# Optimization experiments

Measured on AMD Instinct MI355X. Metric: run time of the kernel, lower is better.

The kernel has to match this reference:

```python
import jax, jax.numpy as jnp
import numpy as np

BN_EPS = 1e-5

def _bn(x, g, b, m, v):
    # eval-mode BatchNorm1d over channel dim of [B, C, N]
    scale = g / jnp.sqrt(v + BN_EPS)
    return (x - m[:, None]) * scale[:, None] + b[:, None]

def _conv1(W, x, b=None):
    # 1x1 Conv1d == channel matmul: W [O, C], x [B, C, N] -> [B, O, N]
    y = jnp.einsum('oc,bcn->bon', W, x)
    if b is not None:
        y = y + b[:, None]
    return y

def _sa_layer(x, wqk, wv, bv, wt, bt, g, b, m, v):
    # offset self-attention; q_conv and k_conv share weights
    xk = _conv1(wqk, x)                          # [B, D, N]
    xq = jnp.swapaxes(xk, 1, 2)                  # [B, N, D]
    xv = _conv1(wv, x, bv)                       # [B, D, N]
    energy = jnp.einsum('bnd,bdm->bnm', xq, xk)  # [B, N, N]
    attn = jax.nn.softmax(energy, axis=-1)
    attn = attn / (1e-9 + attn.sum(axis=1, keepdims=True))  # L1 renorm over dim=1
    x_r = jnp.einsum('bdn,bnm->bdm', xv, attn)   # [B, D, N]
    x_r = jax.nn.relu(_bn(_conv1(wt, x - x_r, bt), g, b, m, v))
    return x + x_r

def setup_inputs() -> dict:
    key = jax.random.key(0)
    ks = iter(jax.random.split(key, 64))
    B, Cin, N = 16, 3, 2048
    D, F, H1, OUT = 128, 1024, 512, 50
    def rn(shape, s=0.05):
        return jax.random.normal(next(ks), shape, dtype=jnp.float32) * s
    def var(shape):
        return jax.random.uniform(next(ks), shape, dtype=jnp.float32) * 0.5 + 0.5
    inp = {
        'x': jax.random.normal(next(ks), (B, Cin, N), dtype=jnp.float32),
        'w1': rn((D, Cin)), 'w2': rn((D, D)),
        'bn1_g': jnp.ones((D,)), 'bn1_b': jnp.zeros((D,)), 'bn1_m': rn((D,)), 'bn1_v': var((D,)),
        'bn2_g': jnp.ones((D,)), 'bn2_b': jnp.zeros((D,)), 'bn2_m': rn((D,)), 'bn2_v': var((D,)),
        'sa_wqk': rn((4, D, D)), 'sa_wv': rn((4, D, D)), 'sa_bv': rn((4, D)),
        'sa_wt': rn((4, D, D)), 'sa_bt': rn((4, D)),
        'sa_g': jnp.ones((4, D)), 'sa_b': jnp.zeros((4, D)), 'sa_m': rn((4, D)), 'sa_v': var((4, D)),
        'wf': rn((F, 4 * D)),
        'bnf_g': jnp.ones((F,)), 'bnf_b': jnp.zeros((F,)), 'bnf_m': rn((F,)), 'bnf_v': var((F,)),
        'ws1': rn((H1, 3 * F)), 'bs1': rn((H1,)),
        'bns1_g': jnp.ones((H1,)), 'bns1_b': jnp.zeros((H1,)), 'bns1_m': rn((H1,)), 'bns1_v': var((H1,)),
        'ws2': rn((OUT, H1)), 'bs2': rn((OUT,)),
        'bns2_g': jnp.ones((OUT,)), 'bns2_b': jnp.zeros((OUT,)), 'bns2_m': rn((OUT,)), 'bns2_v': var((OUT,)),
    }
    return inp

def reference(x, w1, w2, bn1_g, bn1_b, bn1_m, bn1_v, bn2_g, bn2_b, bn2_m, bn2_v,
              sa_wqk, sa_wv, sa_bv, sa_wt, sa_bt, sa_g, sa_b, sa_m, sa_v,
              wf, bnf_g, bnf_b, bnf_m, bnf_v,
              ws1, bs1, bns1_g, bns1_b, bns1_m, bns1_v,
              ws2, bs2, bns2_g, bns2_b, bns2_m, bns2_v):
    B, _, N = x.shape
    h = jax.nn.relu(_bn(_conv1(w1, x), bn1_g, bn1_b, bn1_m, bn1_v))
    h = jax.nn.relu(_bn(_conv1(w2, h), bn2_g, bn2_b, bn2_m, bn2_v))
    feats = []
    for i in range(4):
        h = _sa_layer(h, sa_wqk[i], sa_wv[i], sa_bv[i], sa_wt[i], sa_bt[i],
                      sa_g[i], sa_b[i], sa_m[i], sa_v[i])
        feats.append(h)
    cat = jnp.concatenate(feats, axis=1)                 # [B, 512, N]
    fused = _bn(_conv1(wf, cat), bnf_g, bnf_b, bnf_m, bnf_v)
    fused = jnp.where(fused >= 0, fused, 0.2 * fused)    # LeakyReLU(0.2)
    x_max = fused.max(axis=2)                            # [B, 1024]
    x_avg = fused.mean(axis=2)                           # [B, 1024]
    gmax = jnp.broadcast_to(x_max[:, :, None], (B, x_max.shape[1], N))
    gavg = jnp.broadcast_to(x_avg[:, :, None], (B, x_avg.shape[1], N))
    h = jnp.concatenate([fused, gmax, gavg], axis=1)     # [B, 3072, N]
    h = jax.nn.relu(_bn(_conv1(ws1, h, bs1), bns1_g, bns1_b, bns1_m, bns1_v))
    # dropout is identity in eval mode
    h = jax.nn.relu(_bn(_conv1(ws2, h, bs2), bns2_g, bns2_b, bns2_m, bns2_v))
    return h  # [B, out_channel, N]
```

## Files before the change

### kernel.cpp

```cpp
#include <hip/hip_runtime.h>
#include <cstdint>
#include <cstddef>

#define B_   16
#define N_   2048
#define D_   128
#define F_   1024
#define H1_  512
#define OUT_ 50

static constexpr float BN_EPS = 1e-5f;

typedef __attribute__((ext_vector_type(8))) short short8;
typedef __attribute__((ext_vector_type(4))) float f32x4;

__device__ inline unsigned short f2bf(float f) {
  union { float f; unsigned u; } v; v.f = f;
  unsigned r = v.u + 0x7fff + ((v.u >> 16) & 1);
  return (unsigned short)(r >> 16);
}

__device__ inline void dma16(const unsigned short* g, unsigned short* l) {
  __builtin_amdgcn_global_load_lds(
      (const __attribute__((address_space(1))) unsigned int*)g,
      (__attribute__((address_space(3))) unsigned int*)l, 16, 0, 0);
}

__global__ void foldw_k(const float* __restrict__ W, int ldW,
                        const float* __restrict__ bias,
                        const float* __restrict__ g, const float* __restrict__ bb,
                        const float* __restrict__ m, const float* __restrict__ v,
                        unsigned short* __restrict__ Wb, float* __restrict__ biasF,
                        int O, int Opad, int K) {
  long i = (long)blockIdx.x * 256 + threadIdx.x;
  if (i >= (long)Opad * K) return;
  int o = (int)(i / K), k = (int)(i % K);
  float sc = 1.f, sh = 0.f;
  if (o < O && g) { sc = g[o] * rsqrtf(v[o] + BN_EPS); sh = bb[o] - m[o] * sc; }
  float w = (o < O) ? W[(long)o * ldW + k] * sc : 0.f;
  Wb[i] = f2bf(w);
  if (k == 0 && biasF) {
    float bf = 0.f;
    if (o < O) bf = (bias ? bias[o] : 0.f) * sc + sh;
    biasF[o] = bf;
  }
}

__global__ void conv1_k(const float* __restrict__ x, const float* __restrict__ w1,
                        const float* __restrict__ g, const float* __restrict__ bb,
                        const float* __restrict__ m, const float* __restrict__ v,
                        unsigned short* __restrict__ h0b) {
  int o = threadIdx.x, n = blockIdx.x, b = blockIdx.y;
  const float* xb = x + (long)b * 3 * N_;
  float val = w1[o * 3 + 0] * xb[n] + w1[o * 3 + 1] * xb[N_ + n] + w1[o * 3 + 2] * xb[2 * N_ + n];
  float sc = g[o] * rsqrtf(v[o] + BN_EPS);
  val = val * sc + (bb[o] - m[o] * sc);
  h0b[((long)b * N_ + n) * D_ + o] = f2bf(fmaxf(val, 0.f));
}

template <int TM>
__global__ __launch_bounds__(256, 4)
void gemm_tok(const unsigned short* __restrict__ Wb, int ldW,
              const unsigned short* __restrict__ A, long sA, int ldA,
              const float* __restrict__ biasF,
              const float* __restrict__ perBO, int ldPBO,
              const float* __restrict__ res, long sRes, int ldRes,
              float* __restrict__ outF, long sOutF, int ldOutF,
              unsigned short* __restrict__ outH, long sOutH, int ldOutH,
              float* __restrict__ pmax, float* __restrict__ psum,
              int K, int act, int flags) {
  constexpr int MT = TM / 32;
  __shared__ unsigned short lAB[TM * 64 + 128 * 64];
  __shared__ float lpm[4][64], lps[4][64];
  unsigned short* lA = lAB;
  unsigned short* lB = lAB + TM * 64;
  unsigned short* lS = lAB;
  int tid = threadIdx.x;
  int n0 = blockIdx.x * TM, o0 = blockIdx.y * 128, b = blockIdx.z;
  int wave = tid >> 6, lane = tid & 63;
  int wr = wave >> 1, wc = wave & 1;
  int quad = lane >> 4, l15 = lane & 15;
  int rowL = lane >> 3;
  int kseg = (lane & 7) ^ rowL;
  const unsigned short* Ab = A + (long)b * sA + (long)n0 * ldA;
  const unsigned short* Wp = Wb + (long)o0 * ldW;

  f32x4 acc[MT][4];
  #pragma unroll
  for (int i = 0; i < MT; ++i)
    #pragma unroll
    for (int j = 0; j < 4; ++j) acc[i][j] = (f32x4){0.f, 0.f, 0.f, 0.f};

  for (int kc = 0; kc < K; kc += 64) {
    #pragma unroll
    for (int t = 0; t < 4; ++t) {
      int chunk = t * 4 + wave;
      dma16(Wp + (long)(chunk * 8 + rowL) * ldW + kc + kseg * 8, &lB[chunk * 512]);
      if (chunk < TM / 8)
        dma16(Ab + (long)(chunk * 8 + rowL) * ldA + kc + kseg * 8, &lA[chunk * 512]);
    }
    __syncthreads();
    #pragma unroll
    for (int kk = 0; kk < 2; ++kk) {
      short8 af[MT], bf[4];
      #pragma unroll
      for (int mt = 0; mt < MT; ++mt) {
        int r = wr * (TM / 2) + mt * 16 + l15;
        af[mt] = *(const short8*)&lA[r * 64 + (((kk * 4 + quad) ^ (l15 & 7)) * 8)];
      }
      #pragma unroll
      for (int ot = 0; ot < 4; ++ot) {
        int r = wc * 64 + ot * 16 + l15;
        bf[ot] = *(const short8*)&lB[r * 64 + (((kk * 4 + quad) ^ (l15 & 7)) * 8)];
      }
      #pragma unroll
      for (int mt = 0; mt < MT; ++mt)
        #pragma unroll
        for (int ot = 0; ot < 4; ++ot)
          acc[mt][ot] = __builtin_amdgcn_mfma_f32_16x16x32_bf16(bf[ot], af[mt], acc[mt][ot], 0, 0, 0);
    }
    __syncthreads();
  }

  bool doPool = (flags & 32) != 0;

  if (!outF) {
    #pragma unroll
    for (int ot = 0; ot < 4; ++ot) {
      int obL = wc * 64 + ot * 16 + quad * 4;
      int ob = o0 + obL;
      float bi[4] = {0.f, 0.f, 0.f, 0.f};
      if (biasF) { float4 t = *(const float4*)&biasF[ob]; bi[0] = t.x; bi[1] = t.y; bi[2] = t.z; bi[3] = t.w; }
      if (perBO) {
        float4 t = *(const float4*)&perBO[(long)b * ldPBO + ob];
        bi[0] += t.x; bi[1] += t.y; bi[2] += t.z; bi[3] += t.w;
      }
      float pm4[4], ps4[4];
      #pragma unroll
      for (int r = 0; r < 4; ++r) { pm4[r] = -1e30f; ps4[r] = 0.f; }
      int g = obL >> 3, go = obL & 7;
      #pragma unroll
      for (int mt = 0; mt < MT; ++mt) {
        int nL = wr * (TM / 2) + mt * 16 + l15;
        unsigned short t4[4];
        #pragma unroll
        for (int r = 0; r < 4; ++r) {
          float val = acc[mt][ot][r] + bi[r];
          if (act == 1)      val = fmaxf(val, 0.f);
          else if (act == 2) val = (val >= 0.f) ? val : 0.2f * val;
          t4[r] = f2bf(val);
          if (doPool) { pm4[r] = fmaxf(pm4[r], val); ps4[r] += val; }
        }
        int gp = (g & 8) | ((g ^ (nL & 7)) & 7);
        *(uint2*)&lS[nL * 128 + gp * 8 + go] = *(uint2*)&t4[0];
      }
      if (doPool) {
        #pragma unroll
        for (int r = 0; r < 4; ++r) {
          float m = pm4[r], s = ps4[r];
          m = fmaxf(m, __shfl_xor(m, 1)); s += __shfl_xor(s, 1);
          m = fmaxf(m, __shfl_xor(m, 2)); s += __shfl_xor(s, 2);
          m = fmaxf(m, __shfl_xor(m, 4)); s += __shfl_xor(s, 4);
          m = fmaxf(m, __shfl_xor(m, 8)); s += __shfl_xor(s, 8);
          if (l15 == 0) { lpm[wave][ot * 16 + quad * 4 + r] = m; lps[wave][ot * 16 + quad * 4 + r] = s; }
        }
      }
    }
    __syncthreads();
    {
      int r0 = tid >> 4, s = tid & 15;
      #pragma unroll
      for (int it = 0; it < TM / 16; ++it) {
        int row = it * 16 + r0;
        int sp = (s & 8) | ((s ^ (row & 7)) & 7);
        short8 v = *(const short8*)&lS[row * 128 + sp * 8];
        *(short8*)&outH[(long)b * sOutH + (long)(n0 + row) * ldOutH + o0 + s * 8] = v;
      }
    }
    if (doPool && tid < 128) {
      int wcx = tid >> 6, ol = tid & 63;
      float m = fmaxf(lpm[wcx][ol], lpm[wcx + 2][ol]);
      float s = lps[wcx][ol] + lps[wcx + 2][ol];
      int o = o0 + wcx * 64 + ol;
      pmax[((long)b * 16 + blockIdx.x) * 1024 + o] = m;
      psum[((long)b * 16 + blockIdx.x) * 1024 + o] = s;
    }
    return;
  }

  #pragma unroll
  for (int ot = 0; ot < 4; ++ot) {
    int ob = o0 + wc * 64 + ot * 16 + quad * 4;
    float bi[4] = {0.f, 0.f, 0.f, 0.f};
    if (biasF) { float4 t = *(const float4*)&biasF[ob]; bi[0] = t.x; bi[1] = t.y; bi[2] = t.z; bi[3] = t.w; }
    if (perBO) {
      float4 t = *(const float4*)&perBO[(long)b * ldPBO + ob];
      bi[0] += t.x; bi[1] += t.y; bi[2] += t.z; bi[3] += t.w;
    }
    #pragma unroll
    for (int mt = 0; mt < MT; ++mt) {
      int n = n0 + wr * (TM / 2) + mt * 16 + l15;
      float vals[4];
      #pragma unroll
      for (int r = 0; r < 4; ++r) {
        float val = acc[mt][ot][r] + bi[r];
        if (act == 1)      val = fmaxf(val, 0.f);
        else if (act == 2) val = (val >= 0.f) ? val : 0.2f * val;
        vals[r] = val;
      }
      if (flags & 16) {
        float4 t = *(const float4*)&res[(long)b * sRes + (long)n * ldRes + ob];
        vals[0] += t.x; vals[1] += t.y; vals[2] += t.z; vals[3] += t.w;
      }
      *(float4*)&outF[(long)b * sOutF + (long)n * ldOutF + ob] = *(float4*)vals;
      {
        unsigned short t[4];
        #pragma unroll
        for (int r = 0; r < 4; ++r) t[r] = f2bf(vals[r]);
        *(uint2*)&outH[(long)b * sOutH + (long)n * ldOutH + ob] = *(uint2*)&t[0];
      }
    }
  }
}

template <int TM>
__global__ __launch_bounds__(256, 4)
void gemm_chan(const unsigned short* __restrict__ Wb, int ldW,
               const unsigned short* __restrict__ A, long sA, int ldA,
               const float* __restrict__ biasF,
               float* __restrict__ outF, long sOutF, int ldOutF,
               unsigned short* __restrict__ outH, long sOutH, int ldOutH,
               int K, int O, int act) {
  constexpr int MT = TM / 32;
  __shared__ unsigned short lA[TM * 64];
  __shared__ unsigned short lB[128 * 64];
  int tid = threadIdx.x;
  int n0 = blockIdx.x * TM, o0 = blockIdx.y * 128, b = blockIdx.z;
  int wave = tid >> 6, lane = tid & 63;
  int wr = wave >> 1, wc = wave & 1;
  int quad = lane >> 4, l15 = lane & 15;
  int rowL = lane >> 3;
  int kseg = (lane & 7) ^ rowL;
  const unsigned short* Ab = A + (long)b * sA + (long)n0 * ldA;
  const unsigned short* Wp = Wb + (long)o0 * ldW;

  f32x4 acc[MT][4];
  #pragma unroll
  for (int i = 0; i < MT; ++i)
    #pragma unroll
    for (int j = 0; j < 4; ++j) acc[i][j] = (f32x4){0.f, 0.f, 0.f, 0.f};

  for (int kc = 0; kc < K; kc += 64) {
    #pragma unroll
    for (int t = 0; t < 4; ++t) {
      int chunk = t * 4 + wave;
      dma16(Wp + (long)(chunk * 8 + rowL) * ldW + kc + kseg * 8, &lB[chunk * 512]);
      if (chunk < TM / 8)
        dma16(Ab + (long)(chunk * 8 + rowL) * ldA + kc + kseg * 8, &lA[chunk * 512]);
    }
    __syncthreads();
    #pragma unroll
    for (int kk = 0; kk < 2; ++kk) {
      short8 af[MT], bf[4];
      #pragma unroll
      for (int mt = 0; mt < MT; ++mt) {
        int r = wr * (TM / 2) + mt * 16 + l15;
        af[mt] = *(const short8*)&lA[r * 64 + (((kk * 4 + quad) ^ (l15 & 7)) * 8)];
      }
      #pragma unroll
      for (int ot = 0; ot < 4; ++ot) {
        int r = wc * 64 + ot * 16 + l15;
        bf[ot] = *(const short8*)&lB[r * 64 + (((kk * 4 + quad) ^ (l15 & 7)) * 8)];
      }
      #pragma unroll
      for (int mt = 0; mt < MT; ++mt)
        #pragma unroll
        for (int ot = 0; ot < 4; ++ot)
          acc[mt][ot] = __builtin_amdgcn_mfma_f32_16x16x32_bf16(af[mt], bf[ot], acc[mt][ot], 0, 0, 0);
    }
    __syncthreads();
  }

  #pragma unroll
  for (int ot = 0; ot < 4; ++ot) {
    int o = o0 + wc * 64 + ot * 16 + l15;
    if (o >= O) continue;
    float bi = biasF ? biasF[o] : 0.f;
    #pragma unroll
    for (int mt = 0; mt < MT; ++mt) {
      int nb = n0 + wr * (TM / 2) + mt * 16 + quad * 4;
      float vals[4];
      #pragma unroll
      for (int r = 0; r < 4; ++r) {
        float val = acc[mt][ot][r] + bi;
        if (act == 1)      val = fmaxf(val, 0.f);
        else if (act == 2) val = (val >= 0.f) ? val : 0.2f * val;
        vals[r] = val;
      }
      if (outF)
        *(float4*)&outF[(long)b * sOutF + (long)o * ldOutF + nb] = *(float4*)vals;
      if (outH) {
        unsigned short t[4];
        #pragma unroll
        for (int r = 0; r < 4; ++r) t[r] = f2bf(vals[r]);
        *(uint2*)&outH[(long)b * sOutH + (long)o * ldOutH + nb] = *(uint2*)&t[0];
      }
    }
  }
}

__global__ __launch_bounds__(256)
void gram_lw(const unsigned short* __restrict__ xk, long sXk,
             float* __restrict__ lw) {
  __shared__ unsigned short lK[64 * 128];
  int tid = threadIdx.x, wave = tid >> 6, lane = tid & 63;
  int quad = lane >> 4, l15 = lane & 15;
  int rowL4 = lane >> 4, s16 = lane & 15;
  int n0 = blockIdx.y * 64, b = blockIdx.x;
  const unsigned short* Kp = xk + (long)b * sXk;
  short8 afr[4];
  {
    const unsigned short* arow = Kp + (long)(n0 + wave * 16 + l15) * 128;
    #pragma unroll
    for (int kf = 0; kf < 4; ++kf) afr[kf] = *(const short8*)(arow + kf * 32 + quad * 8);
  }
  float runm[4], runs[4];
  #pragma unroll
  for (int r = 0; r < 4; ++r) { runm[r] = -1e30f; runs[r] = 0.f; }

  for (int m0 = 0; m0 < 2048; m0 += 64) {
    __syncthreads();
    #pragma unroll
    for (int t = 0; t < 4; ++t) {
      int c = t * 4 + wave;
      int row = c * 4 + rowL4;
      int gseg = (s16 & 8) | ((s16 ^ (row & 7)) & 7);
      dma16(Kp + (long)(m0 + row) * 128 + gseg * 8, &lK[c * 512]);
    }
    __syncthreads();
    #pragma unroll
    for (int mf = 0; mf < 4; ++mf) {
      f32x4 s = (f32x4){0.f, 0.f, 0.f, 0.f};
      #pragma unroll
      for (int kf = 0; kf < 4; ++kf) {
        int r = mf * 16 + l15, q = kf * 4 + quad;
        int sp = (q & 8) | ((q ^ (r & 7)) & 7);
        short8 bfr = *(const short8*)&lK[r * 128 + sp * 8];
        s = __builtin_amdgcn_mfma_f32_16x16x32_bf16(afr[kf], bfr, s, 0, 0, 0);
      }
      #pragma unroll
      for (int r = 0; r < 4; ++r) {
        float e = s[r];
        float mn = fmaxf(runm[r], e);
        runs[r] = runs[r] * __expf(runm[r] - mn) + __expf(e - mn);
        runm[r] = mn;
      }
    }
  }
  #pragma unroll
  for (int r = 0; r < 4; ++r) {
    float m = runm[r], s = runs[r];
    #pragma unroll
    for (int off = 1; off < 16; off <<= 1) {
      float mo = __shfl_xor(m, off), so = __shfl_xor(s, off);
      float mn = fmaxf(m, mo);
      s = s * __expf(m - mn) + so * __expf(mo - mn);
      m = mn;
    }
    if (l15 == 0) {
      int n = n0 + wave * 16 + quad * 4 + r;
      lw[(long)b * 2048 + n] = m + __logf(s);
    }
  }
}

__global__ __launch_bounds__(256)
void pv_k(const unsigned short* __restrict__ xk, long sXk,
          const unsigned short* __restrict__ xv, long sXv,
          const float* __restrict__ lw,
          const float* __restrict__ li, long sLi, int ldLi,
          unsigned short* __restrict__ xrb, long sXr) {
  __shared__ unsigned short lK[64 * 128];
  __shared__ unsigned short lV[128 * 64];
  __shared__ unsigned short lP[4][16 * 68];
  __shared__ float lwt[64];
  int tid = threadIdx.x, wave = tid >> 6, lane = tid & 63;
  int quad = lane >> 4, l15 = lane & 15;
  int rowL4 = lane >> 4, s16 = lane & 15;
  int rowL8 = lane >> 3, s8 = lane & 7;
  int m0 = blockIdx.y * 64, b = blockIdx.x;
  const unsigned short* Kp = xk + (long)b * sXk;
  const unsigned short* Vp = xv + (long)b * sXv;
  short8 akr[4];
  {
    const unsigned short* arow = Kp + (long)(m0 + wave * 16 + l15) * 128;
    #pragma unroll
    for (int kf = 0; kf < 4; ++kf) akr[kf] = *(const short8*)(arow + kf * 32 + quad * 8);
  }
  f32x4 acc[8];
  #pragma unroll
  for (int dt = 0; dt < 8; ++dt) acc[dt] = (f32x4){0.f, 0.f, 0.f, 0.f};
  float runc[4] = {0.f, 0.f, 0.f, 0.f};

  for (int n0c = 0; n0c < 2048; n0c += 64) {
    __syncthreads();
    #pragma unroll
    for (int t = 0; t < 4; ++t) {
      int cK = t * 4 + wave;
      int rowK = cK * 4 + rowL4;
      int gsegK = (s16 & 8) | ((s16 ^ (rowK & 7)) & 7);
      dma16(Kp + (long)(n0c + rowK) * 128 + gsegK * 8, &lK[cK * 512]);
      int cV = t * 4 + wave;
      int rowV = cV * 8 + rowL8;
      int gsegV = s8 ^ (rowV & 7);
      dma16(Vp + (long)rowV * 2048 + n0c + gsegV * 8, &lV[cV * 512]);
    }
    if (tid < 64) lwt[tid] = lw[(long)b * 2048 + n0c + tid];
    __syncthreads();
    #pragma unroll
    for (int nf = 0; nf < 4; ++nf) {
      f32x4 s = (f32x4){0.f, 0.f, 0.f, 0.f};
      #pragma unroll
      for (int kf = 0; kf < 4; ++kf) {
        int r = nf * 16 + l15, q = kf * 4 + quad;
        int sp = (q & 8) | ((q ^ (r & 7)) & 7);
        short8 bfr = *(const short8*)&lK[r * 128 + sp * 8];
        s = __builtin_amdgcn_mfma_f32_16x16x32_bf16(akr[kf], bfr, s, 0, 0, 0);
      }
      float lwc = lwt[nf * 16 + l15];
      #pragma unroll
      for (int r = 0; r < 4; ++r) {
        float p = __expf(s[r] - lwc);
        runc[r] += p;
        lP[wave][(quad * 4 + r) * 68 + nf * 16 + l15] = f2bf(p);
      }
    }
    __syncthreads();
    #pragma unroll
    for (int kc = 0; kc < 2; ++kc) {
      short8 pa = *(const short8*)&lP[wave][l15 * 68 + kc * 32 + quad * 8];
      #pragma unroll
      for (int dt = 0; dt < 8; ++dt) {
        int r = dt * 16 + l15, q = kc * 4 + quad;
        int sp = q ^ (r & 7);
        short8 vb = *(const short8*)&lV[r * 64 + sp * 8];
        acc[dt] = __builtin_amdgcn_mfma_f32_16x16x32_bf16(pa, vb, acc[dt], 0, 0, 0);
      }
    }
  }
  float inv[4];
  #pragma unroll
  for (int r = 0; r < 4; ++r) {
    float s = runc[r];
    #pragma unroll
    for (int off = 1; off < 16; off <<= 1) s += __shfl_xor(s, off);
    inv[r] = 1.f / (1e-9f + s);
  }
  #pragma unroll
  for (int dt = 0; dt < 8; ++dt) {
    int d = dt * 16 + l15;
    #pragma unroll
    for (int r = 0; r < 4; ++r) {
      int m = m0 + wave * 16 + quad * 4 + r;
      float lv = li[(long)b * sLi + (long)m * ldLi + d];
      xrb[(long)b * sXr + (long)m * 128 + d] = f2bf(lv - acc[dt][r] * inv[r]);
    }
  }
}

__global__ void poolred_k(const float* __restrict__ pmax, const float* __restrict__ psum,
                          float* __restrict__ xmax, float* __restrict__ xavg) {
  int f = blockIdx.x * 256 + threadIdx.x, b = blockIdx.y;
  float mx = -1e30f, s = 0.f;
  #pragma unroll
  for (int t = 0; t < 16; ++t) {
    mx = fmaxf(mx, pmax[((long)b * 16 + t) * 1024 + f]);
    s += psum[((long)b * 16 + t) * 1024 + f];
  }
  xmax[(long)b * 1024 + f] = mx;
  xavg[(long)b * 1024 + f] = s * (1.f / 2048.f);
}

__global__ __launch_bounds__(256)
void poolterm_k(const float* __restrict__ ws1, const float* __restrict__ xmax,
                const float* __restrict__ xavg,
                const float* __restrict__ bg, const float* __restrict__ bv,
                float* __restrict__ pt) {
  int o = blockIdx.x, b = blockIdx.y, tid = threadIdx.x;
  const float* w = ws1 + (long)o * 3072;
  float s = 0.f;
  #pragma unroll
  for (int it = 0; it < 4; ++it) {
    int c = tid + it * 256;
    s += w[1024 + c] * xmax[(long)b * 1024 + c] + w[2048 + c] * xavg[(long)b * 1024 + c];
  }
  #pragma unroll
  for (int off = 32; off; off >>= 1) s += __shfl_xor(s, off);
  __shared__ float rsm[4];
  if ((tid & 63) == 0) rsm[tid >> 6] = s;
  __syncthreads();
  if (tid == 0) {
    float sc = bg[o] * rsqrtf(bv[o] + BN_EPS);
    pt[(long)b * H1_ + o] = sc * (rsm[0] + rsm[1] + rsm[2] + rsm[3]);
  }
}

extern "C" void kernel_launch(void* const* d_in, const int* in_sizes, int n_in,
                              void* d_out, int out_size, void* d_ws, size_t ws_size,
                              hipStream_t stream) {
  const float* x      = (const float*)d_in[0];
  const float* w1     = (const float*)d_in[1];
  const float* w2     = (const float*)d_in[2];
  const float* bn1_g  = (const float*)d_in[3];
  const float* bn1_b  = (const float*)d_in[4];
  const float* bn1_m  = (const float*)d_in[5];
  const float* bn1_v  = (const float*)d_in[6];
  const float* bn2_g  = (const float*)d_in[7];
  const float* bn2_b  = (const float*)d_in[8];
  const float* bn2_m  = (const float*)d_in[9];
  const float* bn2_v  = (const float*)d_in[10];
  const float* sa_wqk = (const float*)d_in[11];
  const float* sa_wv  = (const float*)d_in[12];
  const float* sa_bv  = (const float*)d_in[13];
  const float* sa_wt  = (const float*)d_in[14];
  const float* sa_bt  = (const float*)d_in[15];
  const float* sa_g   = (const float*)d_in[16];
  const float* sa_b   = (const float*)d_in[17];
  const float* sa_m   = (const float*)d_in[18];
  const float* sa_v   = (const float*)d_in[19];
  const float* wf     = (const float*)d_in[20];
  const float* bnf_g  = (const float*)d_in[21];
  const float* bnf_b  = (const float*)d_in[22];
  const float* bnf_m  = (const float*)d_in[23];
  const float* bnf_v  = (const float*)d_in[24];
  const float* ws1    = (const float*)d_in[25];
  const float* bs1    = (const float*)d_in[26];
  const float* bns1_g = (const float*)d_in[27];
  const float* bns1_b = (const float*)d_in[28];
  const float* bns1_m = (const float*)d_in[29];
  const float* bns1_v = (const float*)d_in[30];
  const float* ws2    = (const float*)d_in[31];
  const float* bs2    = (const float*)d_in[32];
  const float* bns2_g = (const float*)d_in[33];
  const float* bns2_b = (const float*)d_in[34];
  const float* bns2_m = (const float*)d_in[35];
  const float* bns2_v = (const float*)d_in[36];
  float* out = (float*)d_out;

  float* ws = (float*)d_ws;
  size_t off = 0;
  auto alloc  = [&](size_t n) { float* p = ws + off; off += (n + 63) & ~(size_t)63; return p; };
  auto allocH = [&](size_t n) { return (unsigned short*)alloc((n + 1) / 2); };

  unsigned short* w2b  = allocH(128 * 128);
  unsigned short* wqkb = allocH(4 * 128 * 128);
  unsigned short* wvb  = allocH(4 * 128 * 128);
  unsigned short* wtb  = allocH(4 * 128 * 128);
  unsigned short* wfb  = allocH((size_t)F_ * 512);
  unsigned short* ws1b = allocH((size_t)H1_ * 1024);
  unsigned short* ws2b = allocH((size_t)128 * 512);
  float* bias_w2 = alloc(128);
  float* bias_v  = alloc(512);
  float* bias_t  = alloc(512);
  float* bias_f  = alloc(1024);
  float* bias_s1 = alloc(512);
  float* bias_s2 = alloc(128);
  float* lwB  = alloc((size_t)16 * 2048);
  float* pmax = alloc((size_t)16 * 16 * 1024);
  float* psum = alloc((size_t)16 * 16 * 1024);
  float* xmaxB = alloc((size_t)16 * 1024);
  float* xavgB = alloc((size_t)16 * 1024);
  float* ptB   = alloc((size_t)16 * 512);
  size_t fixedOff = off;

  const size_t perB = 262144 + 1048576 + 131072 + 524288 + 1048576 +
                      131072 + 131072 + 131072;
  size_t wsFloats = ws_size / 4;
  int Gb = 1;
  for (int c : {16, 8, 4, 2, 1}) {
    if (fixedOff + (size_t)c * perB + 4096 <= wsFloats) { Gb = c; break; }
  }

  float* h1    = alloc((size_t)Gb * 262144);
  float* feats = alloc((size_t)Gb * 1048576);
  unsigned short* h1b    = allocH((size_t)Gb * 262144);
  unsigned short* featsb = allocH((size_t)Gb * 1048576);
  unsigned short* fusedb = allocH((size_t)Gb * 2097152);
  unsigned short* xkb    = allocH((size_t)Gb * 262144);
  unsigned short* xvb    = allocH((size_t)Gb * 262144);
  unsigned short* xrb    = allocH((size_t)Gb * 262144);
  unsigned short* h0b  = xrb;
  unsigned short* hs1b = featsb;

  foldw_k<<<64, 256, 0, stream>>>(w2, 128, nullptr, bn2_g, bn2_b, bn2_m, bn2_v,
                                  w2b, bias_w2, 128, 128, 128);
  for (int i = 0; i < 4; ++i) {
    foldw_k<<<64, 256, 0, stream>>>(sa_wqk + (size_t)i * 16384, 128, nullptr,
                                    nullptr, nullptr, nullptr, nullptr,
                                    wqkb + (size_t)i * 16384, nullptr, 128, 128, 128);
    foldw_k<<<64, 256, 0, stream>>>(sa_wv + (size_t)i * 16384, 128, sa_bv + i * 128,
                                    nullptr, nullptr, nullptr, nullptr,
                                    wvb + (size_t)i * 16384, bias_v + i * 128, 128, 128, 128);
    foldw_k<<<64, 256, 0, stream>>>(sa_wt + (size_t)i * 16384, 128, sa_bt + i * 128,
                                    sa_g + i * 128, sa_b + i * 128, sa_m + i * 128, sa_v + i * 128,
                                    wtb + (size_t)i * 16384, bias_t + i * 128, 128, 128, 128);
  }
  foldw_k<<<2048, 256, 0, stream>>>(wf, 512, nullptr, bnf_g, bnf_b, bnf_m, bnf_v,
                                    wfb, bias_f, 1024, 1024, 512);
  foldw_k<<<2048, 256, 0, stream>>>(ws1, 3072, bs1, bns1_g, bns1_b, bns1_m, bns1_v,
                                    ws1b, bias_s1, 512, 512, 1024);
  foldw_k<<<256, 256, 0, stream>>>(ws2, 512, bs2, bns2_g, bns2_b, bns2_m, bns2_v,
                                   ws2b, bias_s2, 50, 128, 512);

  const long sAct = 262144, sFeat = 1048576, sFus = 2097152;
  for (int b0 = 0; b0 < B_; b0 += Gb) {
    int g = Gb;
    conv1_k<<<dim3(N_, g), 128, 0, stream>>>(x + (long)b0 * 3 * N_, w1,
                                             bn1_g, bn1_b, bn1_m, bn1_v, h0b);
    gemm_tok<64><<<dim3(32, 1, g), 256, 0, stream>>>(
        w2b, 128, h0b, sAct, 128, bias_w2, nullptr, 0, nullptr, 0, 0,
        h1, sAct, 128, h1b, sAct, 128, nullptr, nullptr, 128, 1, 1);

    for (int i = 0; i < 4; ++i) {
      const unsigned short* lib = (i == 0) ? h1b : featsb + (size_t)(i - 1) * 128;
      const float* liF = (i == 0) ? h1 : feats + (size_t)(i - 1) * 128;
      int ldLi = (i == 0) ? 128 : 512;
      long sLi = (i == 0) ? sAct : sFeat;
      gemm_tok<64><<<dim3(32, 1, g), 256, 0, stream>>>(
          wqkb + (size_t)i * 16384, 128, lib, sLi, ldLi, nullptr, nullptr, 0,
          nullptr, 0, 0, nullptr, 0, 0, xkb, sAct, 128, nullptr, nullptr, 128, 0, 0);
      gemm_chan<64><<<dim3(32, 1, g), 256, 0, stream>>>(
          wvb + (size_t)i * 16384, 128, lib, sLi, ldLi, bias_v + i * 128,
          nullptr, 0, 0, xvb, sAct, 2048, 128, 128, 0);
      gram_lw<<<dim3(g, 32), 256, 0, stream>>>(xkb, sAct, lwB);
      pv_k<<<dim3(g, 32), 256, 0, stream>>>(xkb, sAct, xvb, sAct, lwB,
                                            liF, sLi, ldLi, xrb, sAct);
      gemm_tok<64><<<dim3(32, 1, g), 256, 0, stream>>>(
          wtb + (size_t)i * 16384, 128, xrb, sAct, 128, bias_t + i * 128, nullptr, 0,
          liF, sLi, ldLi,
          feats + (size_t)i * 128, sFeat, 512,
          featsb + (size_t)i * 128, sFeat, 512, nullptr, nullptr, 128, 1, 1 | 16);
    }

    gemm_tok<128><<<dim3(16, 8, g), 256, 0, stream>>>(
        wfb, 512, featsb, sFeat, 512, bias_f, nullptr, 0, nullptr, 0, 0,
        nullptr, 0, 0, fusedb, sFus, 1024, pmax, psum, 512, 2, 32);
    poolred_k<<<dim3(4, g), 256, 0, stream>>>(pmax, psum, xmaxB, xavgB);
    poolterm_k<<<dim3(512, g), 256, 0, stream>>>(ws1, xmaxB, xavgB, bns1_g, bns1_v, ptB);
    gemm_tok<128><<<dim3(16, 4, g), 256, 0, stream>>>(
        ws1b, 1024, fusedb, sFus, 1024, bias_s1, ptB, 512, nullptr, 0, 0,
        nullptr, 0, 0, hs1b, sFeat, 512, nullptr, nullptr, 1024, 1, 0);
    gemm_chan<64><<<dim3(32, 1, g), 256, 0, stream>>>(
        ws2b, 512, hs1b, sFeat, 512, bias_s2,
        out + (long)b0 * OUT_ * N_, (long)OUT_ * N_, 2048, nullptr, 0, 0,
        512, 50, 1);
  }
}
```

Measured before the change: 827.2 us.

## Drop fp32 activation copies, double-buffer attention kernels, swizzle P tile

```diff
diff --git a/kernel.cpp b/kernel.cpp
--- a/kernel.cpp
+++ b/kernel.cpp
@@ -18,6 +18,9 @@
   union { float f; unsigned u; } v; v.f = f;
   unsigned r = v.u + 0x7fff + ((v.u >> 16) & 1);
   return (unsigned short)(r >> 16);
+}
+__device__ inline float bf2f(unsigned short h) {
+  union { unsigned u; float f; } v; v.u = ((unsigned)h) << 16; return v.f;
 }
 
 __device__ inline void dma16(const unsigned short* g, unsigned short* l) {
@@ -64,8 +67,7 @@
               const unsigned short* __restrict__ A, long sA, int ldA,
               const float* __restrict__ biasF,
               const float* __restrict__ perBO, int ldPBO,
-              const float* __restrict__ res, long sRes, int ldRes,
-              float* __restrict__ outF, long sOutF, int ldOutF,
+              const unsigned short* __restrict__ resH, long sRes, int ldRes,
               unsigned short* __restrict__ outH, long sOutH, int ldOutH,
               float* __restrict__ pmax, float* __restrict__ psum,
               int K, int act, int flags) {
@@ -123,83 +125,23 @@
   }
 
   bool doPool = (flags & 32) != 0;
-
-  if (!outF) {
-    #pragma unroll
-    for (int ot = 0; ot < 4; ++ot) {
-      int obL = wc * 64 + ot * 16 + quad * 4;
-      int ob = o0 + obL;
-      float bi[4] = {0.f, 0.f, 0.f, 0.f};
-      if (biasF) { float4 t = *(const float4*)&biasF[ob]; bi[0] = t.x; bi[1] = t.y; bi[2] = t.z; bi[3] = t.w; }
-      if (perBO) {
-        float4 t = *(const float4*)&perBO[(long)b * ldPBO + ob];
-        bi[0] += t.x; bi[1] += t.y; bi[2] += t.z; bi[3] += t.w;
-      }
-      float pm4[4], ps4[4];
-      #pragma unroll
-      for (int r = 0; r < 4; ++r) { pm4[r] = -1e30f; ps4[r] = 0.f; }
-      int g = obL >> 3, go = obL & 7;
-      #pragma unroll
-      for (int mt = 0; mt < MT; ++mt) {
-        int nL = wr * (TM / 2) + mt * 16 + l15;
-        unsigned short t4[4];
-        #pragma unroll
-        for (int r = 0; r < 4; ++r) {
-          float val = acc[mt][ot][r] + bi[r];
-          if (act == 1)      val = fmaxf(val, 0.f);
-          else if (act == 2) val = (val >= 0.f) ? val : 0.2f * val;
-          t4[r] = f2bf(val);
-          if (doPool) { pm4[r] = fmaxf(pm4[r], val); ps4[r] += val; }
-        }
-        int gp = (g & 8) | ((g ^ (nL & 7)) & 7);
-        *(uint2*)&lS[nL * 128 + gp * 8 + go] = *(uint2*)&t4[0];
-      }
-      if (doPool) {
-        #pragma unroll
-        for (int r = 0; r < 4; ++r) {
-          float m = pm4[r], s = ps4[r];
-          m = fmaxf(m, __shfl_xor(m, 1)); s += __shfl_xor(s, 1);
-          m = fmaxf(m, __shfl_xor(m, 2)); s += __shfl_xor(s, 2);
-          m = fmaxf(m, __shfl_xor(m, 4)); s += __shfl_xor(s, 4);
-          m = fmaxf(m, __shfl_xor(m, 8)); s += __shfl_xor(s, 8);
-          if (l15 == 0) { lpm[wave][ot * 16 + quad * 4 + r] = m; lps[wave][ot * 16 + quad * 4 + r] = s; }
-        }
-      }
-    }
-    __syncthreads();
-    {
-      int r0 = tid >> 4, s = tid & 15;
-      #pragma unroll
-      for (int it = 0; it < TM / 16; ++it) {
-        int row = it * 16 + r0;
-        int sp = (s & 8) | ((s ^ (row & 7)) & 7);
-        short8 v = *(const short8*)&lS[row * 128 + sp * 8];
-        *(short8*)&outH[(long)b * sOutH + (long)(n0 + row) * ldOutH + o0 + s * 8] = v;
-      }
-    }
-    if (doPool && tid < 128) {
-      int wcx = tid >> 6, ol = tid & 63;
-      float m = fmaxf(lpm[wcx][ol], lpm[wcx + 2][ol]);
-      float s = lps[wcx][ol] + lps[wcx + 2][ol];
-      int o = o0 + wcx * 64 + ol;
-      pmax[((long)b * 16 + blockIdx.x) * 1024 + o] = m;
-      psum[((long)b * 16 + blockIdx.x) * 1024 + o] = s;
-    }
-    return;
-  }
-
   #pragma unroll
   for (int ot = 0; ot < 4; ++ot) {
-    int ob = o0 + wc * 64 + ot * 16 + quad * 4;
+    int obL = wc * 64 + ot * 16 + quad * 4;
+    int ob = o0 + obL;
     float bi[4] = {0.f, 0.f, 0.f, 0.f};
     if (biasF) { float4 t = *(const float4*)&biasF[ob]; bi[0] = t.x; bi[1] = t.y; bi[2] = t.z; bi[3] = t.w; }
     if (perBO) {
       float4 t = *(const float4*)&perBO[(long)b * ldPBO + ob];
       bi[0] += t.x; bi[1] += t.y; bi[2] += t.z; bi[3] += t.w;
     }
+    float pm4[4], ps4[4];
+    #pragma unroll
+    for (int r = 0; r < 4; ++r) { pm4[r] = -1e30f; ps4[r] = 0.f; }
+    int g = obL >> 3, go = obL & 7;
     #pragma unroll
     for (int mt = 0; mt < MT; ++mt) {
-      int n = n0 + wr * (TM / 2) + mt * 16 + l15;
+      int nL = wr * (TM / 2) + mt * 16 + l15;
       float vals[4];
       #pragma unroll
       for (int r = 0; r < 4; ++r) {
@@ -209,17 +151,51 @@
         vals[r] = val;
       }
       if (flags & 16) {
-        float4 t = *(const float4*)&res[(long)b * sRes + (long)n * ldRes + ob];
-        vals[0] += t.x; vals[1] += t.y; vals[2] += t.z; vals[3] += t.w;
-      }
-      *(float4*)&outF[(long)b * sOutF + (long)n * ldOutF + ob] = *(float4*)vals;
-      {
-        unsigned short t[4];
+        uint2 rv = *(const uint2*)&resH[(long)b * sRes + (long)(n0 + nL) * ldRes + ob];
+        unsigned short rr[4];
+        *(uint2*)rr = rv;
         #pragma unroll
-        for (int r = 0; r < 4; ++r) t[r] = f2bf(vals[r]);
-        *(uint2*)&outH[(long)b * sOutH + (long)n * ldOutH + ob] = *(uint2*)&t[0];
-      }
-    }
+        for (int r = 0; r < 4; ++r) vals[r] += bf2f(rr[r]);
+      }
+      unsigned short t4[4];
+      #pragma unroll
+      for (int r = 0; r < 4; ++r) {
+        t4[r] = f2bf(vals[r]);
+        if (doPool) { pm4[r] = fmaxf(pm4[r], vals[r]); ps4[r] += vals[r]; }
+      }
+      int gp = (g & 8) | ((g ^ (nL & 7)) & 7);
+      *(uint2*)&lS[nL * 128 + gp * 8 + go] = *(uint2*)&t4[0];
+    }
+    if (doPool) {
+      #pragma unroll
+      for (int r = 0; r < 4; ++r) {
+        float m = pm4[r], s = ps4[r];
+        m = fmaxf(m, __shfl_xor(m, 1)); s += __shfl_xor(s, 1);
+        m = fmaxf(m, __shfl_xor(m, 2)); s += __shfl_xor(s, 2);
+        m = fmaxf(m, __shfl_xor(m, 4)); s += __shfl_xor(s, 4);
+        m = fmaxf(m, __shfl_xor(m, 8)); s += __shfl_xor(s, 8);
+        if (l15 == 0) { lpm[wave][ot * 16 + quad * 4 + r] = m; lps[wave][ot * 16 + quad * 4 + r] = s; }
+      }
+    }
+  }
+  __syncthreads();
+  {
+    int r0 = tid >> 4, s = tid & 15;
+    #pragma unroll
+    for (int it = 0; it < TM / 16; ++it) {
+      int row = it * 16 + r0;
+      int sp = (s & 8) | ((s ^ (row & 7)) & 7);
+      short8 v = *(const short8*)&lS[row * 128 + sp * 8];
+      *(short8*)&outH[(long)b * sOutH + (long)(n0 + row) * ldOutH + o0 + s * 8] = v;
+    }
+  }
+  if (doPool && tid < 128) {
+    int wcx = tid >> 6, ol = tid & 63;
+    float m = fmaxf(lpm[wcx][ol], lpm[wcx + 2][ol]);
+    float s = lps[wcx][ol] + lps[wcx + 2][ol];
+    int o = o0 + wcx * 64 + ol;
+    pmax[((long)b * 16 + blockIdx.x) * 1024 + o] = m;
+    psum[((long)b * 16 + blockIdx.x) * 1024 + o] = s;
   }
 }
 
@@ -312,7 +288,7 @@
 __global__ __launch_bounds__(256)
 void gram_lw(const unsigned short* __restrict__ xk, long sXk,
              float* __restrict__ lw) {
-  __shared__ unsigned short lK[64 * 128];
+  __shared__ unsigned short lK[2][64 * 128];
   int tid = threadIdx.x, wave = tid >> 6, lane = tid & 63;
   int quad = lane >> 4, l15 = lane & 15;
   int rowL4 = lane >> 4, s16 = lane & 15;
@@ -328,16 +304,22 @@
   #pragma unroll
   for (int r = 0; r < 4; ++r) { runm[r] = -1e30f; runs[r] = 0.f; }
 
-  for (int m0 = 0; m0 < 2048; m0 += 64) {
-    __syncthreads();
+  auto stage = [&](int ch, int bf) {
     #pragma unroll
     for (int t = 0; t < 4; ++t) {
       int c = t * 4 + wave;
       int row = c * 4 + rowL4;
       int gseg = (s16 & 8) | ((s16 ^ (row & 7)) & 7);
-      dma16(Kp + (long)(m0 + row) * 128 + gseg * 8, &lK[c * 512]);
-    }
+      dma16(Kp + (long)(ch * 64 + row) * 128 + gseg * 8, &lK[bf][c * 512]);
+    }
+  };
+  stage(0, 0);
+
+  for (int ch = 0; ch < 32; ++ch) {
     __syncthreads();
+    int bf = ch & 1;
+    if (ch + 1 < 32) stage(ch + 1, bf ^ 1);
+    f32x4 sv[4];
     #pragma unroll
     for (int mf = 0; mf < 4; ++mf) {
       f32x4 s = (f32x4){0.f, 0.f, 0.f, 0.f};
@@ -345,16 +327,19 @@
       for (int kf = 0; kf < 4; ++kf) {
         int r = mf * 16 + l15, q = kf * 4 + quad;
         int sp = (q & 8) | ((q ^ (r & 7)) & 7);
-        short8 bfr = *(const short8*)&lK[r * 128 + sp * 8];
+        short8 bfr = *(const short8*)&lK[bf][r * 128 + sp * 8];
         s = __builtin_amdgcn_mfma_f32_16x16x32_bf16(afr[kf], bfr, s, 0, 0, 0);
       }
-      #pragma unroll
-      for (int r = 0; r < 4; ++r) {
-        float e = s[r];
-        float mn = fmaxf(runm[r], e);
-        runs[r] = runs[r] * __expf(runm[r] - mn) + __expf(e - mn);
-        runm[r] = mn;
-      }
+      sv[mf] = s;
+    }
+    #pragma unroll
+    for (int r = 0; r < 4; ++r) {
+      float e0 = sv[0][r], e1 = sv[1][r], e2 = sv[2][r], e3 = sv[3][r];
+      float cm = fmaxf(fmaxf(e0, e1), fmaxf(e2, e3));
+      float mn = fmaxf(runm[r], cm);
+      runs[r] = runs[r] * __expf(runm[r] - mn) +
+                (__expf(e0 - mn) + __expf(e1 - mn)) + (__expf(e2 - mn) + __expf(e3 - mn));
+      runm[r] = mn;
     }
   }
   #pragma unroll
@@ -378,12 +363,12 @@
 void pv_k(const unsigned short* __restrict__ xk, long sXk,
           const unsigned short* __restrict__ xv, long sXv,
           const float* __restrict__ lw,
-          const float* __restrict__ li, long sLi, int ldLi,
+          const unsigned short* __restrict__ lib, long sLi, int ldLi,
           unsigned short* __restrict__ xrb, long sXr) {
-  __shared__ unsigned short lK[64 * 128];
-  __shared__ unsigned short lV[128 * 64];
-  __shared__ unsigned short lP[4][16 * 68];
-  __shared__ float lwt[64];
+  __shared__ unsigned short lK[2][64 * 128];
+  __shared__ unsigned short lV[2][128 * 64];
+  __shared__ unsigned short lP[4][16 * 64];
+  __shared__ float lwt[2][64];
   int tid = threadIdx.x, wave = tid >> 6, lane = tid & 63;
   int quad = lane >> 4, l15 = lane & 15;
   int rowL4 = lane >> 4, s16 = lane & 15;
@@ -402,21 +387,25 @@
   for (int dt = 0; dt < 8; ++dt) acc[dt] = (f32x4){0.f, 0.f, 0.f, 0.f};
   float runc[4] = {0.f, 0.f, 0.f, 0.f};
 
-  for (int n0c = 0; n0c < 2048; n0c += 64) {
+  auto stage = [&](int ch, int bf) {
+    #pragma unroll
+    for (int t = 0; t < 4; ++t) {
+      int c = t * 4 + wave;
+      int rowK = c * 4 + rowL4;
+      int gsegK = (s16 & 8) | ((s16 ^ (rowK & 7)) & 7);
+      dma16(Kp + (long)(ch * 64 + rowK) * 128 + gsegK * 8, &lK[bf][c * 512]);
+      int rowV = c * 8 + rowL8;
+      int gsegV = s8 ^ (rowV & 7);
+      dma16(Vp + (long)rowV * 2048 + ch * 64 + gsegV * 8, &lV[bf][c * 512]);
+    }
+    if (tid < 64) lwt[bf][tid] = lw[(long)b * 2048 + ch * 64 + tid];
+  };
+  stage(0, 0);
+
+  for (int ch = 0; ch < 32; ++ch) {
     __syncthreads();
-    #pragma unroll
-    for (int t = 0; t < 4; ++t) {
-      int cK = t * 4 + wave;
-      int rowK = cK * 4 + rowL4;
-      int gsegK = (s16 & 8) | ((s16 ^ (rowK & 7)) & 7);
-      dma16(Kp + (long)(n0c + rowK) * 128 + gsegK * 8, &lK[cK * 512]);
-      int cV = t * 4 + wave;
-      int rowV = cV * 8 + rowL8;
-      int gsegV = s8 ^ (rowV & 7);
-      dma16(Vp + (long)rowV * 2048 + n0c + gsegV * 8, &lV[cV * 512]);
-    }
-    if (tid < 64) lwt[tid] = lw[(long)b * 2048 + n0c + tid];
-    __syncthreads();
+    int bf = ch & 1;
+    if (ch + 1 < 32) stage(ch + 1, bf ^ 1);
     #pragma unroll
     for (int nf = 0; nf < 4; ++nf) {
       f32x4 s = (f32x4){0.f, 0.f, 0.f, 0.f};
@@ -424,26 +413,29 @@
       for (int kf = 0; kf < 4; ++kf) {
         int r = nf * 16 + l15, q = kf * 4 + quad;
         int sp = (q & 8) | ((q ^ (r & 7)) & 7);
-        short8 bfr = *(const short8*)&lK[r * 128 + sp * 8];
+        short8 bfr = *(const short8*)&lK[bf][r * 128 + sp * 8];
         s = __builtin_amdgcn_mfma_f32_16x16x32_bf16(akr[kf], bfr, s, 0, 0, 0);
       }
-      float lwc = lwt[nf * 16 + l15];
+      float lwc = lwt[bf][nf * 16 + l15];
+      int segIn = nf * 2 + (l15 >> 3);
       #pragma unroll
       for (int r = 0; r < 4; ++r) {
         float p = __expf(s[r] - lwc);
         runc[r] += p;
-        lP[wave][(quad * 4 + r) * 68 + nf * 16 + l15] = f2bf(p);
-      }
-    }
-    __syncthreads();
+        int row = quad * 4 + r;
+        int seg = (segIn ^ (row & 7)) & 7;
+        lP[wave][row * 64 + seg * 8 + (l15 & 7)] = f2bf(p);
+      }
+    }
     #pragma unroll
     for (int kc = 0; kc < 2; ++kc) {
-      short8 pa = *(const short8*)&lP[wave][l15 * 68 + kc * 32 + quad * 8];
+      int qp = kc * 4 + quad;
+      short8 pa = *(const short8*)&lP[wave][l15 * 64 + ((qp ^ (l15 & 7)) & 7) * 8];
       #pragma unroll
       for (int dt = 0; dt < 8; ++dt) {
-        int r = dt * 16 + l15, q = kc * 4 + quad;
-        int sp = q ^ (r & 7);
-        short8 vb = *(const short8*)&lV[r * 64 + sp * 8];
+        int r = dt * 16 + l15;
+        int sp = qp ^ (r & 7);
+        short8 vb = *(const short8*)&lV[bf][r * 64 + sp * 8];
         acc[dt] = __builtin_amdgcn_mfma_f32_16x16x32_bf16(pa, vb, acc[dt], 0, 0, 0);
       }
     }
@@ -462,7 +454,7 @@
     #pragma unroll
     for (int r = 0; r < 4; ++r) {
       int m = m0 + wave * 16 + quad * 4 + r;
-      float lv = li[(long)b * sLi + (long)m * ldLi + d];
+      float lv = bf2f(lib[(long)b * sLi + (long)m * ldLi + d]);
       xrb[(long)b * sXr + (long)m * 128 + d] = f2bf(lv - acc[dt][r] * inv[r]);
     }
   }
@@ -573,16 +565,13 @@
   float* ptB   = alloc((size_t)16 * 512);
   size_t fixedOff = off;
 
-  const size_t perB = 262144 + 1048576 + 131072 + 524288 + 1048576 +
-                      131072 + 131072 + 131072;
+  const size_t perB = 131072 + 524288 + 1048576 + 131072 + 131072 + 131072;
   size_t wsFloats = ws_size / 4;
   int Gb = 1;
   for (int c : {16, 8, 4, 2, 1}) {
     if (fixedOff + (size_t)c * perB + 4096 <= wsFloats) { Gb = c; break; }
   }
 
-  float* h1    = alloc((size_t)Gb * 262144);
-  float* feats = alloc((size_t)Gb * 1048576);
   unsigned short* h1b    = allocH((size_t)Gb * 262144);
   unsigned short* featsb = allocH((size_t)Gb * 1048576);
   unsigned short* fusedb = allocH((size_t)Gb * 2097152);
@@ -619,37 +608,35 @@
                                              bn1_g, bn1_b, bn1_m, bn1_v, h0b);
     gemm_tok<64><<<dim3(32, 1, g), 256, 0, stream>>>(
         w2b, 128, h0b, sAct, 128, bias_w2, nullptr, 0, nullptr, 0, 0,
-        h1, sAct, 128, h1b, sAct, 128, nullptr, nullptr, 128, 1, 1);
+        h1b, sAct, 128, nullptr, nullptr, 128, 1, 0);
 
     for (int i = 0; i < 4; ++i) {
       const unsigned short* lib = (i == 0) ? h1b : featsb + (size_t)(i - 1) * 128;
-      const float* liF = (i == 0) ? h1 : feats + (size_t)(i - 1) * 128;
       int ldLi = (i == 0) ? 128 : 512;
       long sLi = (i == 0) ? sAct : sFeat;
       gemm_tok<64><<<dim3(32, 1, g), 256, 0, stream>>>(
           wqkb + (size_t)i * 16384, 128, lib, sLi, ldLi, nullptr, nullptr, 0,
-          nullptr, 0, 0, nullptr, 0, 0, xkb, sAct, 128, nullptr, nullptr, 128, 0, 0);
+          nullptr, 0, 0, xkb, sAct, 128, nullptr, nullptr, 128, 0, 0);
       gemm_chan<64><<<dim3(32, 1, g), 256, 0, stream>>>(
           wvb + (size_t)i * 16384, 128, lib, sLi, ldLi, bias_v + i * 128,
           nullptr, 0, 0, xvb, sAct, 2048, 128, 128, 0);
       gram_lw<<<dim3(g, 32), 256, 0, stream>>>(xkb, sAct, lwB);
       pv_k<<<dim3(g, 32), 256, 0, stream>>>(xkb, sAct, xvb, sAct, lwB,
-                                            liF, sLi, ldLi, xrb, sAct);
+                                            lib, sLi, ldLi, xrb, sAct);
       gemm_tok<64><<<dim3(32, 1, g), 256, 0, stream>>>(
           wtb + (size_t)i * 16384, 128, xrb, sAct, 128, bias_t + i * 128, nullptr, 0,
-          liF, sLi, ldLi,
-          feats + (size_t)i * 128, sFeat, 512,
-          featsb + (size_t)i * 128, sFeat, 512, nullptr, nullptr, 128, 1, 1 | 16);
+          lib, sLi, ldLi,
+          featsb + (size_t)i * 128, sFeat, 512, nullptr, nullptr, 128, 1, 16);
     }
 
     gemm_tok<128><<<dim3(16, 8, g), 256, 0, stream>>>(
         wfb, 512, featsb, sFeat, 512, bias_f, nullptr, 0, nullptr, 0, 0,
-        nullptr, 0, 0, fusedb, sFus, 1024, pmax, psum, 512, 2, 32);
+        fusedb, sFus, 1024, pmax, psum, 512, 2, 32);
     poolred_k<<<dim3(4, g), 256, 0, stream>>>(pmax, psum, xmaxB, xavgB);
     poolterm_k<<<dim3(512, g), 256, 0, stream>>>(ws1, xmaxB, xavgB, bns1_g, bns1_v, ptB);
     gemm_tok<128><<<dim3(16, 4, g), 256, 0, stream>>>(
         ws1b, 1024, fusedb, sFus, 1024, bias_s1, ptB, 512, nullptr, 0, 0,
-        nullptr, 0, 0, hs1b, sFeat, 512, nullptr, nullptr, 1024, 1, 0);
+        hs1b, sFeat, 512, nullptr, nullptr, 1024, 1, 0);
     gemm_chan<64><<<dim3(32, 1, g), 256, 0, stream>>>(
         ws2b, 512, hs1b, sFeat, 512, bias_s2,
         out + (long)b0 * OUT_ * N_, (long)OUT_ * N_, 2048, nullptr, 0, 0,
```

Measured after the change: 782.6 us. -5.4%, faster.
